# Optimization experiments

Measured on AMD Instinct MI355X. Metric: run time of the kernel, lower is better.

## Reference

```python
import jax, jax.numpy as jnp
import numpy as np

B, S, D = 8, 2048, 1024


def setup_inputs() -> dict:
    key = jax.random.key(0)
    ks = jax.random.split(key, 9)
    scale = 1.0 / np.sqrt(D)
    inp = {
        "query": jax.random.normal(ks[0], (B, S, D), dtype=jnp.float32),
        "key": jax.random.normal(ks[1], (B, S, D), dtype=jnp.float32),
        "value": jax.random.normal(ks[2], (B, S, D), dtype=jnp.float32),
        # causal boolean mask, broadcast over batch; True = keep, False = -inf
        "mask": jnp.tril(jnp.ones((S, S), dtype=bool)),
        "Wq": jax.random.normal(ks[3], (D, D), dtype=jnp.float32) * scale,
        "bq": jax.random.normal(ks[4], (D,), dtype=jnp.float32) * 0.02,
        "Wk": jax.random.normal(ks[5], (D, D), dtype=jnp.float32) * scale,
        "bk": jax.random.normal(ks[6], (D,), dtype=jnp.float32) * 0.02,
        "Wv": jax.random.normal(ks[7], (D, D), dtype=jnp.float32) * scale,
        "bv": jax.random.normal(ks[8], (D,), dtype=jnp.float32) * 0.02,
    }
    return inp


def reference(query, key, value, mask, Wq, bq, Wk, bk, Wv, bv):
    dk = Wq.shape[1]
    # linear projections: nn.Linear stores weight as [out,in]; here W is [in,out]
    q = jnp.einsum("bsd,de->bse", query, Wq) + bq
    k = jnp.einsum("bsd,de->bse", key, Wk) + bk
    v = jnp.einsum("bsd,de->bse", value, Wv) + bv
    # scaled dot-product scores [B, S, S]
    scores = jnp.einsum("bqd,bkd->bqk", q, k) / jnp.sqrt(jnp.asarray(dk, q.dtype))
    scores = jnp.where(mask, scores, jnp.asarray(-jnp.inf, scores.dtype))
    attn = jax.nn.softmax(scores, axis=-1)
    return jnp.einsum("bqk,bkd->bqd", attn, v)
```

## Files before the change

kernel.cpp:

```cpp
#include <hip/hip_runtime.h>

#define BB 8
#define SS 2048
#define DD 1024
#define BK 32

typedef unsigned short u16;
typedef __bf16 bf16x8 __attribute__((ext_vector_type(8)));
typedef float f32x4 __attribute__((ext_vector_type(4)));

__device__ __forceinline__ u16 f2bf(float f) {
  unsigned int u = __builtin_bit_cast(unsigned int, f);
  u += 0x7fffu + ((u >> 16) & 1u);
  return (u16)(u >> 16);
}
__device__ __forceinline__ float bf2f(u16 h) {
  unsigned int u = ((unsigned int)h) << 16;
  return __builtin_bit_cast(float, u);
}

__device__ __forceinline__ void gl2lds16(const u16* g, u16* l) {
  __builtin_amdgcn_global_load_lds(
      (const __attribute__((address_space(1))) unsigned int*)g,
      (__attribute__((address_space(3))) unsigned int*)l, 16, 0, 0);
}

__device__ __forceinline__ void stage_tile(const u16* gbase, size_t gstride,
                                           u16* lds, int wave, int lane) {
#pragma unroll
  for (int r = 0; r < 2; r++) {
    int rowblk = r * 64 + wave * 16;
    int row = rowblk + (lane >> 2);
    int col = (lane & 3) * 8;
    gl2lds16(gbase + (size_t)row * gstride + col, lds + rowblk * BK);
  }
}

__global__ void convert_bf16(const float* __restrict__ q, const float* __restrict__ k,
                             const float* __restrict__ v, u16* __restrict__ Xall) {
  int z = blockIdx.y;
  const float* x = (z == 0) ? q : (z == 1) ? k : v;
  u16* y = Xall + (size_t)z * (BB * SS * DD);
  size_t i = (size_t)blockIdx.x * 256 + threadIdx.x;
  const float4* s = (const float4*)x;
  float4 a = s[2 * i], b = s[2 * i + 1];
  uint4 p;
  p.x = (unsigned)f2bf(a.x) | ((unsigned)f2bf(a.y) << 16);
  p.y = (unsigned)f2bf(a.z) | ((unsigned)f2bf(a.w) << 16);
  p.z = (unsigned)f2bf(b.x) | ((unsigned)f2bf(b.y) << 16);
  p.w = (unsigned)f2bf(b.z) | ((unsigned)f2bf(b.w) << 16);
  ((uint4*)y)[i] = p;
}

__global__ void wt_transpose(const float* __restrict__ Wq, const float* __restrict__ Wk,
                             const float* __restrict__ Wv, u16* __restrict__ Wall) {
  __shared__ u16 t[32][33];
  int z = blockIdx.z & 3;
  const float* W = (z == 0) ? Wq : (z == 1) ? Wk : Wv;
  u16* Wt = Wall + (size_t)z * (DD * DD);
  int n0 = blockIdx.x * 32, k0 = blockIdx.y * 32;
  int tx = threadIdx.x & 31, ty = threadIdx.x >> 5;
#pragma unroll
  for (int i = 0; i < 32; i += 8)
    t[ty + i][tx] = f2bf(W[(size_t)(k0 + ty + i) * DD + n0 + tx]);
  __syncthreads();
#pragma unroll
  for (int i = 0; i < 32; i += 8)
    Wt[(size_t)(n0 + ty + i) * DD + k0 + tx] = t[tx][ty + i];
}

__global__ void vt_transpose(const u16* __restrict__ Vsd, u16* __restrict__ Vds) {
  __shared__ u16 t[32][33];
  int b = blockIdx.z;
  int d0 = blockIdx.x * 32, s0 = blockIdx.y * 32;
  const u16* src = Vsd + (size_t)b * SS * DD;
  u16* dst = Vds + (size_t)b * SS * DD;
  int tx = threadIdx.x & 31, ty = threadIdx.x >> 5;
#pragma unroll
  for (int i = 0; i < 32; i += 8)
    t[ty + i][tx] = src[(size_t)(s0 + ty + i) * DD + d0 + tx];
  __syncthreads();
#pragma unroll
  for (int i = 0; i < 32; i += 8)
    dst[(size_t)(d0 + ty + i) * SS + s0 + tx] = t[tx][ty + i];
}

__device__ __forceinline__ void mfma_tile(const u16* As, const u16* Bs, int wm, int wn,
                                          int quad, int l16, f32x4 (&acc)[4][4]) {
  bf16x8 a[4], b[4];
#pragma unroll
  for (int i = 0; i < 4; i++)
    a[i] = *reinterpret_cast<const bf16x8*>(&As[(wm + i * 16 + l16) * BK + quad * 8]);
#pragma unroll
  for (int j = 0; j < 4; j++)
    b[j] = *reinterpret_cast<const bf16x8*>(&Bs[(wn + j * 16 + l16) * BK + quad * 8]);
#pragma unroll
  for (int i = 0; i < 4; i++)
#pragma unroll
    for (int j = 0; j < 4; j++)
      acc[i][j] = __builtin_amdgcn_mfma_f32_16x16x32_bf16(a[i], b[j], acc[i][j], 0, 0, 0);
}

__global__ void proj_gemm(const u16* __restrict__ Xall, const u16* __restrict__ Wall,
                          const float* __restrict__ bq, const float* __restrict__ bk,
                          const float* __restrict__ bv, u16* __restrict__ QKV) {
  __shared__ __align__(16) u16 As[128 * BK];
  __shared__ __align__(16) u16 Bs[128 * BK];
  int id = blockIdx.x;
  int z = id >> 10, rem = id & 1023;
  int r = rem & 7, j = rem >> 3;
  int bn = j & 7, bm = ((j >> 3) << 3) | r;
  const u16* Xb = Xall + (size_t)z * (BB * SS * DD);
  const u16* Wt = Wall + (size_t)z * (DD * DD);
  const float* bias = (z == 0) ? bq : (z == 1) ? bk : bv;
  u16* Out = QKV + (size_t)z * (BB * SS * DD);
  int m0 = bm * 128, n0 = bn * 128;
  int tid = threadIdx.x;
  int lane = tid & 63, wave = tid >> 6;
  int wm = (wave >> 1) * 64, wn = (wave & 1) * 64;
  int quad = lane >> 4, l16 = lane & 15;

  f32x4 acc[4][4];
  f32x4 zz = {0.f, 0.f, 0.f, 0.f};
#pragma unroll
  for (int i = 0; i < 4; i++)
#pragma unroll
    for (int jj = 0; jj < 4; jj++) acc[i][jj] = zz;

  for (int k0 = 0; k0 < DD; k0 += BK) {
    __syncthreads();
    stage_tile(Xb + (size_t)m0 * DD + k0, DD, As, wave, lane);
    stage_tile(Wt + (size_t)n0 * DD + k0, DD, Bs, wave, lane);
    __syncthreads();
    mfma_tile(As, Bs, wm, wn, quad, l16, acc);
  }
#pragma unroll
  for (int i = 0; i < 4; i++) {
#pragma unroll
    for (int rr = 0; rr < 4; rr++) {
      int row = m0 + wm + i * 16 + quad * 4 + rr;
#pragma unroll
      for (int jj = 0; jj < 4; jj++) {
        int col = n0 + wn + jj * 16 + l16;
        Out[(size_t)row * DD + col] = f2bf(acc[i][jj][rr] + bias[col]);
      }
    }
  }
}

__global__ void scores_gemm(const u16* __restrict__ Q, const u16* __restrict__ Kp,
                            u16* __restrict__ Sc) {
  __shared__ __align__(16) u16 As[128 * BK];
  __shared__ __align__(16) u16 Bs[128 * BK];
  int id = blockIdx.x;
  int b = id & 7, t = id >> 3;
  int bm = (int)((sqrtf(8.f * t + 1.f) - 1.f) * 0.5f);
  while ((bm + 1) * (bm + 2) / 2 <= t) bm++;
  while (bm * (bm + 1) / 2 > t) bm--;
  int bn = t - bm * (bm + 1) / 2;

  const u16* Qb = Q + (size_t)b * SS * DD;
  const u16* Kb = Kp + (size_t)b * SS * DD;
  u16* Sb = Sc + (size_t)b * SS * SS;
  int m0 = bm * 128, n0 = bn * 128;
  int tid = threadIdx.x;
  int lane = tid & 63, wave = tid >> 6;
  int wm = (wave >> 1) * 64, wn = (wave & 1) * 64;
  int quad = lane >> 4, l16 = lane & 15;

  f32x4 acc[4][4];
  f32x4 z = {0.f, 0.f, 0.f, 0.f};
#pragma unroll
  for (int i = 0; i < 4; i++)
#pragma unroll
    for (int jj = 0; jj < 4; jj++) acc[i][jj] = z;

  for (int k0 = 0; k0 < DD; k0 += BK) {
    __syncthreads();
    stage_tile(Qb + (size_t)m0 * DD + k0, DD, As, wave, lane);
    stage_tile(Kb + (size_t)n0 * DD + k0, DD, Bs, wave, lane);
    __syncthreads();
    mfma_tile(As, Bs, wm, wn, quad, l16, acc);
  }
#pragma unroll
  for (int i = 0; i < 4; i++) {
#pragma unroll
    for (int rr = 0; rr < 4; rr++) {
      int gi = m0 + wm + i * 16 + quad * 4 + rr;
#pragma unroll
      for (int jj = 0; jj < 4; jj++) {
        int gj = n0 + wn + jj * 16 + l16;
        if (gj <= gi) Sb[(size_t)gi * SS + gj] = f2bf(acc[i][jj][rr] * 0.03125f);
      }
    }
  }
}

__global__ void softmax_causal(const u16* __restrict__ Sc, u16* __restrict__ P) {
  int i = blockIdx.x, b = blockIdx.y;
  const u16* srow = Sc + ((size_t)b * SS + i) * SS;
  u16* prow = P + ((size_t)b * SS + i) * SS;
  int n = i + 1;
  int nceil = ((i >> 7) + 1) << 7;
  int tid = threadIdx.x;
  int lane = tid & 63, wave = tid >> 6;
  __shared__ float sm[4];
  __shared__ float ssum[4];

  int j0 = tid * 8;
  bool act = j0 < nceil;
  float v[8];
  float mx = -3.0e38f;
  if (act) {
    uint4 raw = ((const uint4*)srow)[tid];
    unsigned w[4] = {raw.x, raw.y, raw.z, raw.w};
#pragma unroll
    for (int u = 0; u < 8; u++) {
      u16 h = (u16)((w[u >> 1] >> ((u & 1) * 16)) & 0xffffu);
      v[u] = (j0 + u < n) ? bf2f(h) : -3.0e38f;
      mx = fmaxf(mx, v[u]);
    }
  } else {
#pragma unroll
    for (int u = 0; u < 8; u++) v[u] = -3.0e38f;
  }
#pragma unroll
  for (int off = 32; off > 0; off >>= 1) mx = fmaxf(mx, __shfl_down(mx, off, 64));
  if (lane == 0) sm[wave] = mx;
  __syncthreads();
  mx = fmaxf(fmaxf(sm[0], sm[1]), fmaxf(sm[2], sm[3]));

  float e[8];
  float sum = 0.f;
#pragma unroll
  for (int u = 0; u < 8; u++) {
    e[u] = __expf(v[u] - mx);
    sum += e[u];
  }
#pragma unroll
  for (int off = 32; off > 0; off >>= 1) sum += __shfl_down(sum, off, 64);
  if (lane == 0) ssum[wave] = sum;
  __syncthreads();
  sum = ssum[0] + ssum[1] + ssum[2] + ssum[3];
  float inv = 1.0f / sum;
  if (act) {
    uint4 o;
    unsigned* ow = (unsigned*)&o;
#pragma unroll
    for (int u = 0; u < 4; u++) {
      u16 lo = f2bf(e[2 * u] * inv);
      u16 hi = f2bf(e[2 * u + 1] * inv);
      ow[u] = (unsigned)lo | ((unsigned)hi << 16);
    }
    ((uint4*)prow)[tid] = o;
  }
}

__global__ void pv_gemm(const u16* __restrict__ P, const u16* __restrict__ Vt,
                        float* __restrict__ O) {
  __shared__ __align__(16) u16 As[64 * BK];
  __shared__ __align__(16) u16 Bs[128 * BK];
  int id = blockIdx.x;
  int bn = id & 7, q = (id >> 3) & 15, b = id >> 7;
  const u16* Pb = P + (size_t)b * SS * SS;
  const u16* Vb = Vt + (size_t)b * SS * DD;
  float* Ob = O + (size_t)b * SS * DD;
  int n0 = bn * 128;
  int tid = threadIdx.x;
  int lane = tid & 63, wave = tid >> 6;
  int wn = wave * 32;
  int quad = lane >> 4, l16 = lane & 15;

#pragma unroll
  for (int phase = 0; phase < 2; phase++) {
    int bm = phase ? (31 - q) : q;
    int m0 = bm * 64;
    f32x4 acc[4][2];
    f32x4 z = {0.f, 0.f, 0.f, 0.f};
#pragma unroll
    for (int i = 0; i < 4; i++)
#pragma unroll
      for (int jj = 0; jj < 2; jj++) acc[i][jj] = z;

    int kmax = (bm + 1) * 64;
    for (int k0 = 0; k0 < kmax; k0 += BK) {
      __syncthreads();
      {
        int row = wave * 16 + (lane >> 2);
        int col = (lane & 3) * 8;
        gl2lds16(Pb + (size_t)(m0 + row) * SS + k0 + col, As + wave * 16 * BK);
      }
      stage_tile(Vb + (size_t)n0 * SS + k0, SS, Bs, wave, lane);
      __syncthreads();
      bf16x8 a[4], bb[2];
#pragma unroll
      for (int i = 0; i < 4; i++)
        a[i] = *reinterpret_cast<const bf16x8*>(&As[(i * 16 + l16) * BK + quad * 8]);
#pragma unroll
      for (int jj = 0; jj < 2; jj++)
        bb[jj] = *reinterpret_cast<const bf16x8*>(&Bs[(wn + jj * 16 + l16) * BK + quad * 8]);
#pragma unroll
      for (int i = 0; i < 4; i++)
#pragma unroll
        for (int jj = 0; jj < 2; jj++)
          acc[i][jj] = __builtin_amdgcn_mfma_f32_16x16x32_bf16(a[i], bb[jj], acc[i][jj], 0, 0, 0);
    }
#pragma unroll
    for (int i = 0; i < 4; i++) {
#pragma unroll
      for (int rr = 0; rr < 4; rr++) {
        int row = m0 + i * 16 + quad * 4 + rr;
#pragma unroll
        for (int jj = 0; jj < 2; jj++) {
          int col = n0 + wn + jj * 16 + l16;
          Ob[(size_t)row * DD + col] = acc[i][jj][rr];
        }
      }
    }
  }
}

extern "C" void kernel_launch(void* const* d_in, const int* in_sizes, int n_in,
                              void* d_out, int out_size, void* d_ws, size_t ws_size,
                              hipStream_t stream) {
  const float* query = (const float*)d_in[0];
  const float* key_ = (const float*)d_in[1];
  const float* value = (const float*)d_in[2];
  const float* Wq = (const float*)d_in[4];
  const float* bq = (const float*)d_in[5];
  const float* Wk = (const float*)d_in[6];
  const float* bk = (const float*)d_in[7];
  const float* Wv = (const float*)d_in[8];
  const float* bv = (const float*)d_in[9];
  float* out = (float*)d_out;
  char* ws = (char*)d_ws;

  const size_t MB = 1048576ull;
  u16* Xall = (u16*)(ws + 0);
  u16* QKV  = (u16*)(ws + 96 * MB);
  u16* Qb   = (u16*)(ws + 96 * MB);
  u16* Kb   = (u16*)(ws + 128 * MB);
  u16* Vb   = (u16*)(ws + 160 * MB);
  u16* Wall = (u16*)(ws + 192 * MB);
  u16* Vt   = (u16*)(ws + 0);
  u16* Sc   = (u16*)(ws + 32 * MB);
  u16* P    = (u16*)(ws + 96 * MB);

  dim3 blk(256, 1, 1);
  wt_transpose<<<dim3(32, 32, 3), blk, 0, stream>>>(Wq, Wk, Wv, Wall);
  convert_bf16<<<dim3(8192, 3, 1), blk, 0, stream>>>(query, key_, value, Xall);
  proj_gemm<<<dim3(3072, 1, 1), blk, 0, stream>>>(Xall, Wall, bq, bk, bv, QKV);
  vt_transpose<<<dim3(32, 64, 8), blk, 0, stream>>>(Vb, Vt);
  scores_gemm<<<dim3(1088, 1, 1), blk, 0, stream>>>(Qb, Kb, Sc);
  softmax_causal<<<dim3(2048, 8, 1), blk, 0, stream>>>(Sc, P);
  pv_gemm<<<dim3(1024, 1, 1), blk, 0, stream>>>(P, Vt, out);
}
```

Measured before the change: 521.4 us.

## Fuse prep kernels, emit transposed V from projection, double K-step per barrier

Merges the fp32->bf16 input conversion and the weight transpose into a single prep launch. The V projection now computes W^T·X^T (operands swapped) so it writes V already transposed, which removes the separate vt_transpose pass over V. All three GEMMs now stage two BK slices per barrier pair, halving the number of synchronisations, at the cost of doubled LDS use per block. The transposed V stores are strided along d, which may coalesce less well than before.

After: 477.6 us. -8.4%, faster.

```diff
diff --git a/kernel.cpp b/kernel.cpp
--- a/kernel.cpp
+++ b/kernel.cpp
@@ -4,6 +4,7 @@
 #define SS 2048
 #define DD 1024
 #define BK 32
+#define TSZ (128 * BK)
 
 typedef unsigned short u16;
 typedef __bf16 bf16x8 __attribute__((ext_vector_type(8)));
@@ -36,55 +37,6 @@
   }
 }
 
-__global__ void convert_bf16(const float* __restrict__ q, const float* __restrict__ k,
-                             const float* __restrict__ v, u16* __restrict__ Xall) {
-  int z = blockIdx.y;
-  const float* x = (z == 0) ? q : (z == 1) ? k : v;
-  u16* y = Xall + (size_t)z * (BB * SS * DD);
-  size_t i = (size_t)blockIdx.x * 256 + threadIdx.x;
-  const float4* s = (const float4*)x;
-  float4 a = s[2 * i], b = s[2 * i + 1];
-  uint4 p;
-  p.x = (unsigned)f2bf(a.x) | ((unsigned)f2bf(a.y) << 16);
-  p.y = (unsigned)f2bf(a.z) | ((unsigned)f2bf(a.w) << 16);
-  p.z = (unsigned)f2bf(b.x) | ((unsigned)f2bf(b.y) << 16);
-  p.w = (unsigned)f2bf(b.z) | ((unsigned)f2bf(b.w) << 16);
-  ((uint4*)y)[i] = p;
-}
-
-__global__ void wt_transpose(const float* __restrict__ Wq, const float* __restrict__ Wk,
-                             const float* __restrict__ Wv, u16* __restrict__ Wall) {
-  __shared__ u16 t[32][33];
-  int z = blockIdx.z & 3;
-  const float* W = (z == 0) ? Wq : (z == 1) ? Wk : Wv;
-  u16* Wt = Wall + (size_t)z * (DD * DD);
-  int n0 = blockIdx.x * 32, k0 = blockIdx.y * 32;
-  int tx = threadIdx.x & 31, ty = threadIdx.x >> 5;
-#pragma unroll
-  for (int i = 0; i < 32; i += 8)
-    t[ty + i][tx] = f2bf(W[(size_t)(k0 + ty + i) * DD + n0 + tx]);
-  __syncthreads();
-#pragma unroll
-  for (int i = 0; i < 32; i += 8)
-    Wt[(size_t)(n0 + ty + i) * DD + k0 + tx] = t[tx][ty + i];
-}
-
-__global__ void vt_transpose(const u16* __restrict__ Vsd, u16* __restrict__ Vds) {
-  __shared__ u16 t[32][33];
-  int b = blockIdx.z;
-  int d0 = blockIdx.x * 32, s0 = blockIdx.y * 32;
-  const u16* src = Vsd + (size_t)b * SS * DD;
-  u16* dst = Vds + (size_t)b * SS * DD;
-  int tx = threadIdx.x & 31, ty = threadIdx.x >> 5;
-#pragma unroll
-  for (int i = 0; i < 32; i += 8)
-    t[ty + i][tx] = src[(size_t)(s0 + ty + i) * DD + d0 + tx];
-  __syncthreads();
-#pragma unroll
-  for (int i = 0; i < 32; i += 8)
-    dst[(size_t)(d0 + ty + i) * SS + s0 + tx] = t[tx][ty + i];
-}
-
 __device__ __forceinline__ void mfma_tile(const u16* As, const u16* Bs, int wm, int wn,
                                           int quad, int l16, f32x4 (&acc)[4][4]) {
   bf16x8 a[4], b[4];
@@ -101,11 +53,49 @@
       acc[i][j] = __builtin_amdgcn_mfma_f32_16x16x32_bf16(a[i], b[j], acc[i][j], 0, 0, 0);
 }
 
+__global__ void prep(const float* __restrict__ q, const float* __restrict__ k,
+                     const float* __restrict__ v, u16* __restrict__ Xall,
+                     const float* __restrict__ Wq, const float* __restrict__ Wk,
+                     const float* __restrict__ Wv, u16* __restrict__ Wall) {
+  __shared__ u16 t[32][33];
+  int id = blockIdx.x;
+  if (id < 24576) {
+    int z = id >> 13;
+    int chunk = id & 8191;
+    const float* x = (z == 0) ? q : (z == 1) ? k : v;
+    u16* y = Xall + (size_t)z * (BB * SS * DD);
+    size_t i = (size_t)chunk * 256 + threadIdx.x;
+    const float4* s = (const float4*)x;
+    float4 a = s[2 * i], b = s[2 * i + 1];
+    uint4 p;
+    p.x = (unsigned)f2bf(a.x) | ((unsigned)f2bf(a.y) << 16);
+    p.y = (unsigned)f2bf(a.z) | ((unsigned)f2bf(a.w) << 16);
+    p.z = (unsigned)f2bf(b.x) | ((unsigned)f2bf(b.y) << 16);
+    p.w = (unsigned)f2bf(b.z) | ((unsigned)f2bf(b.w) << 16);
+    ((uint4*)y)[i] = p;
+  } else {
+    int tt = id - 24576;
+    int z = tt >> 10, t2 = tt & 1023;
+    const float* W = (z == 0) ? Wq : (z == 1) ? Wk : Wv;
+    u16* Wt = Wall + (size_t)z * (DD * DD);
+    int n0 = (t2 & 31) * 32, k0 = (t2 >> 5) * 32;
+    int tx = threadIdx.x & 31, ty = threadIdx.x >> 5;
+#pragma unroll
+    for (int i = 0; i < 32; i += 8)
+      t[ty + i][tx] = f2bf(W[(size_t)(k0 + ty + i) * DD + n0 + tx]);
+    __syncthreads();
+#pragma unroll
+    for (int i = 0; i < 32; i += 8)
+      Wt[(size_t)(n0 + ty + i) * DD + k0 + tx] = t[tx][ty + i];
+  }
+}
+
 __global__ void proj_gemm(const u16* __restrict__ Xall, const u16* __restrict__ Wall,
                           const float* __restrict__ bq, const float* __restrict__ bk,
-                          const float* __restrict__ bv, u16* __restrict__ QKV) {
-  __shared__ __align__(16) u16 As[128 * BK];
-  __shared__ __align__(16) u16 Bs[128 * BK];
+                          const float* __restrict__ bv, u16* __restrict__ QK,
+                          u16* __restrict__ Vt) {
+  __shared__ __align__(16) u16 As[2 * TSZ];
+  __shared__ __align__(16) u16 Bs[2 * TSZ];
   int id = blockIdx.x;
   int z = id >> 10, rem = id & 1023;
   int r = rem & 7, j = rem >> 3;
@@ -113,13 +103,15 @@
   const u16* Xb = Xall + (size_t)z * (BB * SS * DD);
   const u16* Wt = Wall + (size_t)z * (DD * DD);
   const float* bias = (z == 0) ? bq : (z == 1) ? bk : bv;
-  u16* Out = QKV + (size_t)z * (BB * SS * DD);
   int m0 = bm * 128, n0 = bn * 128;
   int tid = threadIdx.x;
   int lane = tid & 63, wave = tid >> 6;
   int wm = (wave >> 1) * 64, wn = (wave & 1) * 64;
   int quad = lane >> 4, l16 = lane & 15;
 
+  const u16* Abase = (z < 2) ? (Xb + (size_t)m0 * DD) : (Wt + (size_t)n0 * DD);
+  const u16* Bbase = (z < 2) ? (Wt + (size_t)n0 * DD) : (Xb + (size_t)m0 * DD);
+
   f32x4 acc[4][4];
   f32x4 zz = {0.f, 0.f, 0.f, 0.f};
 #pragma unroll
@@ -127,22 +119,43 @@
 #pragma unroll
     for (int jj = 0; jj < 4; jj++) acc[i][jj] = zz;
 
-  for (int k0 = 0; k0 < DD; k0 += BK) {
-    __syncthreads();
-    stage_tile(Xb + (size_t)m0 * DD + k0, DD, As, wave, lane);
-    stage_tile(Wt + (size_t)n0 * DD + k0, DD, Bs, wave, lane);
+  for (int k0 = 0; k0 < DD; k0 += 2 * BK) {
+    __syncthreads();
+    stage_tile(Abase + k0, DD, As, wave, lane);
+    stage_tile(Abase + k0 + BK, DD, As + TSZ, wave, lane);
+    stage_tile(Bbase + k0, DD, Bs, wave, lane);
+    stage_tile(Bbase + k0 + BK, DD, Bs + TSZ, wave, lane);
     __syncthreads();
     mfma_tile(As, Bs, wm, wn, quad, l16, acc);
-  }
-#pragma unroll
-  for (int i = 0; i < 4; i++) {
-#pragma unroll
-    for (int rr = 0; rr < 4; rr++) {
-      int row = m0 + wm + i * 16 + quad * 4 + rr;
-#pragma unroll
-      for (int jj = 0; jj < 4; jj++) {
-        int col = n0 + wn + jj * 16 + l16;
-        Out[(size_t)row * DD + col] = f2bf(acc[i][jj][rr] + bias[col]);
+    mfma_tile(As + TSZ, Bs + TSZ, wm, wn, quad, l16, acc);
+  }
+  if (z < 2) {
+    u16* Out = QK + (size_t)z * (BB * SS * DD);
+#pragma unroll
+    for (int i = 0; i < 4; i++) {
+#pragma unroll
+      for (int rr = 0; rr < 4; rr++) {
+        int row = m0 + wm + i * 16 + quad * 4 + rr;
+#pragma unroll
+        for (int jj = 0; jj < 4; jj++) {
+          int col = n0 + wn + jj * 16 + l16;
+          Out[(size_t)row * DD + col] = f2bf(acc[i][jj][rr] + bias[col]);
+        }
+      }
+    }
+  } else {
+    int b = m0 >> 11, s0 = m0 & 2047;
+#pragma unroll
+    for (int i = 0; i < 4; i++) {
+#pragma unroll
+      for (int rr = 0; rr < 4; rr++) {
+        int d = n0 + wm + i * 16 + quad * 4 + rr;
+        float bd = bias[d];
+#pragma unroll
+        for (int jj = 0; jj < 4; jj++) {
+          int s = s0 + wn + jj * 16 + l16;
+          Vt[((size_t)b * DD + d) * SS + s] = f2bf(acc[i][jj][rr] + bd);
+        }
       }
     }
   }
@@ -150,8 +163,8 @@
 
 __global__ void scores_gemm(const u16* __restrict__ Q, const u16* __restrict__ Kp,
                             u16* __restrict__ Sc) {
-  __shared__ __align__(16) u16 As[128 * BK];
-  __shared__ __align__(16) u16 Bs[128 * BK];
+  __shared__ __align__(16) u16 As[2 * TSZ];
+  __shared__ __align__(16) u16 Bs[2 * TSZ];
   int id = blockIdx.x;
   int b = id & 7, t = id >> 3;
   int bm = (int)((sqrtf(8.f * t + 1.f) - 1.f) * 0.5f);
@@ -175,12 +188,15 @@
 #pragma unroll
     for (int jj = 0; jj < 4; jj++) acc[i][jj] = z;
 
-  for (int k0 = 0; k0 < DD; k0 += BK) {
+  for (int k0 = 0; k0 < DD; k0 += 2 * BK) {
     __syncthreads();
     stage_tile(Qb + (size_t)m0 * DD + k0, DD, As, wave, lane);
+    stage_tile(Qb + (size_t)m0 * DD + k0 + BK, DD, As + TSZ, wave, lane);
     stage_tile(Kb + (size_t)n0 * DD + k0, DD, Bs, wave, lane);
+    stage_tile(Kb + (size_t)n0 * DD + k0 + BK, DD, Bs + TSZ, wave, lane);
     __syncthreads();
     mfma_tile(As, Bs, wm, wn, quad, l16, acc);
+    mfma_tile(As + TSZ, Bs + TSZ, wm, wn, quad, l16, acc);
   }
 #pragma unroll
   for (int i = 0; i < 4; i++) {
@@ -258,8 +274,8 @@
 
 __global__ void pv_gemm(const u16* __restrict__ P, const u16* __restrict__ Vt,
                         float* __restrict__ O) {
-  __shared__ __align__(16) u16 As[64 * BK];
-  __shared__ __align__(16) u16 Bs[128 * BK];
+  __shared__ __align__(16) u16 As[2 * 64 * BK];
+  __shared__ __align__(16) u16 Bs[2 * TSZ];
   int id = blockIdx.x;
   int bn = id & 7, q = (id >> 3) & 15, b = id >> 7;
   const u16* Pb = P + (size_t)b * SS * SS;
@@ -283,27 +299,35 @@
       for (int jj = 0; jj < 2; jj++) acc[i][jj] = z;
 
     int kmax = (bm + 1) * 64;
-    for (int k0 = 0; k0 < kmax; k0 += BK) {
+    for (int k0 = 0; k0 < kmax; k0 += 2 * BK) {
       __syncthreads();
-      {
+#pragma unroll
+      for (int sub = 0; sub < 2; sub++) {
         int row = wave * 16 + (lane >> 2);
         int col = (lane & 3) * 8;
-        gl2lds16(Pb + (size_t)(m0 + row) * SS + k0 + col, As + wave * 16 * BK);
+        gl2lds16(Pb + (size_t)(m0 + row) * SS + k0 + sub * BK + col,
+                 As + sub * 64 * BK + wave * 16 * BK);
       }
       stage_tile(Vb + (size_t)n0 * SS + k0, SS, Bs, wave, lane);
+      stage_tile(Vb + (size_t)n0 * SS + k0 + BK, SS, Bs + TSZ, wave, lane);
       __syncthreads();
-      bf16x8 a[4], bb[2];
-#pragma unroll
-      for (int i = 0; i < 4; i++)
-        a[i] = *reinterpret_cast<const bf16x8*>(&As[(i * 16 + l16) * BK + quad * 8]);
-#pragma unroll
-      for (int jj = 0; jj < 2; jj++)
-        bb[jj] = *reinterpret_cast<const bf16x8*>(&Bs[(wn + jj * 16 + l16) * BK + quad * 8]);
-#pragma unroll
-      for (int i = 0; i < 4; i++)
+#pragma unroll
+      for (int sub = 0; sub < 2; sub++) {
+        const u16* Asub = As + sub * 64 * BK;
+        const u16* Bsub = Bs + sub * TSZ;
+        bf16x8 a[4], bb[2];
+#pragma unroll
+        for (int i = 0; i < 4; i++)
+          a[i] = *reinterpret_cast<const bf16x8*>(&Asub[(i * 16 + l16) * BK + quad * 8]);
 #pragma unroll
         for (int jj = 0; jj < 2; jj++)
-          acc[i][jj] = __builtin_amdgcn_mfma_f32_16x16x32_bf16(a[i], bb[jj], acc[i][jj], 0, 0, 0);
+          bb[jj] = *reinterpret_cast<const bf16x8*>(&Bsub[(wn + jj * 16 + l16) * BK + quad * 8]);
+#pragma unroll
+        for (int i = 0; i < 4; i++)
+#pragma unroll
+          for (int jj = 0; jj < 2; jj++)
+            acc[i][jj] = __builtin_amdgcn_mfma_f32_16x16x32_bf16(a[i], bb[jj], acc[i][jj], 0, 0, 0);
+      }
     }
 #pragma unroll
     for (int i = 0; i < 4; i++) {
@@ -337,20 +361,17 @@
 
   const size_t MB = 1048576ull;
   u16* Xall = (u16*)(ws + 0);
-  u16* QKV  = (u16*)(ws + 96 * MB);
+  u16* QK   = (u16*)(ws + 96 * MB);
   u16* Qb   = (u16*)(ws + 96 * MB);
   u16* Kb   = (u16*)(ws + 128 * MB);
-  u16* Vb   = (u16*)(ws + 160 * MB);
+  u16* Vt   = (u16*)(ws + 160 * MB);
   u16* Wall = (u16*)(ws + 192 * MB);
-  u16* Vt   = (u16*)(ws + 0);
   u16* Sc   = (u16*)(ws + 32 * MB);
   u16* P    = (u16*)(ws + 96 * MB);
 
   dim3 blk(256, 1, 1);
-  wt_transpose<<<dim3(32, 32, 3), blk, 0, stream>>>(Wq, Wk, Wv, Wall);
-  convert_bf16<<<dim3(8192, 3, 1), blk, 0, stream>>>(query, key_, value, Xall);
-  proj_gemm<<<dim3(3072, 1, 1), blk, 0, stream>>>(Xall, Wall, bq, bk, bv, QKV);
-  vt_transpose<<<dim3(32, 64, 8), blk, 0, stream>>>(Vb, Vt);
+  prep<<<dim3(27648, 1, 1), blk, 0, stream>>>(query, key_, value, Xall, Wq, Wk, Wv, Wall);
+  proj_gemm<<<dim3(3072, 1, 1), blk, 0, stream>>>(Xall, Wall, bq, bk, bv, QK, Vt);
   scores_gemm<<<dim3(1088, 1, 1), blk, 0, stream>>>(Qb, Kb, Sc);
   softmax_causal<<<dim3(2048, 8, 1), blk, 0, stream>>>(Sc, P);
   pv_gemm<<<dim3(1024, 1, 1), blk, 0, stream>>>(P, Vt, out);
```
